# Performance work log

Hardware: AMD Instinct MI355X
Metric: run time of the kernel (lower is better)

Reference implementation:

```python
import jax, jax.numpy as jnp
import numpy as np

B, Lq, Lk, D, H = 8, 1024, 1024, 1024, 16
HD = D // H  # 64


def rotate_half(x):
    x1, x2 = jnp.split(x, 2, axis=-1)
    return jnp.concatenate([-x2, x1], axis=-1)


def setup_inputs() -> dict:
    key = jax.random.key(0)
    ks = jax.random.split(key, 16)
    inv_freq = 1.0 / (10000.0 ** (np.arange(0, HD, 2, dtype=np.float32) / HD))
    pos = np.arange(Lk, dtype=np.float32)
    ang = pos[:, None] * inv_freq[None, :]              # [Lk, HD/2]
    emb = np.concatenate([ang, ang], axis=-1)           # [Lk, HD]
    rope_cos = jnp.broadcast_to(jnp.asarray(np.cos(emb)), (B, Lk, HD))
    rope_sin = jnp.broadcast_to(jnp.asarray(np.sin(emb)), (B, Lk, HD))
    w = lambda k: jax.random.normal(k, (D, D), jnp.float32) * 0.02
    return {
        "query": jax.random.normal(ks[0], (B, Lq, D), jnp.float32),
        "key": jax.random.normal(ks[1], (B, Lk, D), jnp.float32),
        "value": jax.random.normal(ks[2], (B, Lk, D), jnp.float32),
        "Wq": w(ks[3]), "bq": jnp.zeros((D,), jnp.float32),
        "Wk": w(ks[4]), "bk": jnp.zeros((D,), jnp.float32),
        "Wv": w(ks[5]), "bv": jnp.zeros((D,), jnp.float32),
        "Wg": w(ks[6]), "bg": jnp.ones((D,), jnp.float32),
        "Wo": w(ks[7]), "bo": jnp.zeros((D,), jnp.float32),
        "rope_cos": rope_cos,
        "rope_sin": rope_sin,
        "key_padding_mask": jnp.zeros((B, Lk), bool),  # True = padded
    }


def reference(query, key, value, Wq, bq, Wk, bk, Wv, bv, Wg, bg, Wo, bo,
              rope_cos, rope_sin, key_padding_mask):
    b, lq, d = query.shape
    lk = key.shape[1]
    h, hd = H, d // H

    def heads(x, L):  # [B,L,D] -> [B,H,L,hd]
        return x.reshape(b, L, h, hd).transpose(0, 2, 1, 3)

    Q = heads(query @ Wq.T + bq, lq)
    K = heads(key @ Wk.T + bk, lk)
    V = heads(value @ Wv.T + bv, lk)

    def rope(x, cos, sin):
        L = x.shape[2]
        c = cos[:, None, :L, :]
        s = sin[:, None, :L, :]
        return x * c + rotate_half(x) * s

    K = rope(K, rope_cos, rope_sin)
    Q = rope(Q, rope_cos, rope_sin)  # rope_on_q=True, q uses same cos/sin

    scale = 1.0 / np.sqrt(hd)
    scores = jnp.einsum('bhqd,bhkd->bhqk', Q, K) * scale
    valid = ~key_padding_mask                     # [B,Lk], True = attend
    scores = jnp.where(valid[:, None, None, :], scores, jnp.float32(-1e30))
    attn = jax.nn.softmax(scores, axis=-1)
    out = jnp.einsum('bhqk,bhkd->bhqd', attn, V)  # [B,H,Lq,hd]
    out = jnp.nan_to_num(out, nan=0.0)
    out = out.transpose(0, 2, 1, 3).reshape(b, lq, d)
    gate = jax.nn.sigmoid(query @ Wg.T + bg)
    out = (out * gate) @ Wo.T + bo
    return out
```

## Files before the change

kernel.cpp:

```cpp
#include <hip/hip_runtime.h>

using ushort  = unsigned short;
using bf16x8  = __attribute__((ext_vector_type(8))) __bf16;
using bf16x4  = __attribute__((ext_vector_type(4))) __bf16;
using ushort8 = __attribute__((ext_vector_type(8))) unsigned short;
using f32x4   = __attribute__((ext_vector_type(4))) float;
using float4v = __attribute__((ext_vector_type(4))) float;

__device__ __forceinline__ float bf2f(ushort u) {
    union { unsigned int i; float f; } v; v.i = ((unsigned int)u) << 16; return v.f;
}
__device__ __forceinline__ ushort f2bf(float f) {
    union { float f; unsigned int i; } v; v.f = f;
    unsigned int r = v.i + 0x7FFFu + ((v.i >> 16) & 1u);
    return (ushort)(r >> 16);
}
__device__ __forceinline__ bf16x8 ld8(const ushort* p) {
    return __builtin_bit_cast(bf16x8, *(const ushort8*)p);
}
__device__ __forceinline__ void glds16(const void* g, void* l) {
    __builtin_amdgcn_global_load_lds(
        (const __attribute__((address_space(1))) unsigned int*)g,
        (__attribute__((address_space(3))) unsigned int*)l, 16, 0, 0);
}

__global__ void sniff_kernel(const ushort* __restrict__ q, int* __restrict__ flag) {
    const int lane = threadIdx.x;
    float mx = 0.0f;
    for (int i = lane; i < 512; i += 64) {
        float v = bf2f(q[2 * i]);
        mx = fmaxf(mx, fabsf(v));
    }
#pragma unroll
    for (int off = 32; off >= 1; off >>= 1) mx = fmaxf(mx, __shfl_xor(mx, off, 64));
    if (lane == 0) *flag = (mx > 1.0e6f) ? 1 : 0;
}

__device__ __forceinline__ void cvt8(const void* src, ushort* dst, int i, bool f32m) {
    if (f32m) {
        const float4v a = ((const float4v*)src)[2 * i];
        const float4v b = ((const float4v*)src)[2 * i + 1];
        bf16x8 o;
#pragma unroll
        for (int j = 0; j < 4; ++j) { o[j] = (__bf16)a[j]; o[j + 4] = (__bf16)b[j]; }
        ((ushort8*)dst)[i] = __builtin_bit_cast(ushort8, o);
    } else {
        ((ushort8*)dst)[i] = ((const ushort8*)src)[i];
    }
}

__global__ __launch_bounds__(256) void cvt_qkv(
    const void* __restrict__ s0, const void* __restrict__ s1, const void* __restrict__ s2,
    ushort* __restrict__ d0, ushort* __restrict__ d1, ushort* __restrict__ d2,
    const int* __restrict__ flag)
{
    const bool f32m = (*flag != 0);
    const int seg = blockIdx.x >> 11;
    const void* src = seg == 0 ? s0 : (seg == 1 ? s1 : s2);
    ushort*    dst = seg == 0 ? d0 : (seg == 1 ? d1 : d2);
    for (int i = (blockIdx.x & 2047) * 256 + threadIdx.x; i < 1048576; i += 2048 * 256)
        cvt8(src, dst, i, f32m);
}
__global__ __launch_bounds__(256) void cvt_w5(
    const void* __restrict__ s0, const void* __restrict__ s1, const void* __restrict__ s2,
    const void* __restrict__ s3, const void* __restrict__ s4,
    ushort* __restrict__ d0, ushort* __restrict__ d1, ushort* __restrict__ d2,
    ushort* __restrict__ d3, ushort* __restrict__ d4,
    const int* __restrict__ flag)
{
    const bool f32m = (*flag != 0);
    const int seg = blockIdx.x >> 9;
    const void* src = seg == 0 ? s0 : seg == 1 ? s1 : seg == 2 ? s2 : seg == 3 ? s3 : s4;
    ushort*    dst = seg == 0 ? d0 : seg == 1 ? d1 : seg == 2 ? d2 : seg == 3 ? d3 : d4;
    cvt8(src, dst, (blockIdx.x & 511) * 256 + threadIdx.x, f32m);
}

#define CHUNK_SWZ(r, s) ((s) ^ (((r) >> 1) & 3))

template<int EPI, int ABF16, int WBF16, int OUTF>
__global__ __launch_bounds__(256) void gemm_bt(
    const void* __restrict__ A, const void* __restrict__ W,
    const void* __restrict__ bias,
    const void* __restrict__ rc, const void* __restrict__ rs,
    void* __restrict__ C, const int* __restrict__ flag)
{
    constexpr int Kd = 1024, Nd = 1024;
    const bool f32m = (*flag != 0);
    const bool af32 = f32m && !ABF16;
    const bool wf32 = f32m && !WBF16;

    const int tid  = threadIdx.x;
    const int swz  = (blockIdx.x & 7) * 64 + (blockIdx.x >> 3);
    const int nb   = swz & 7;
    const int mb   = swz >> 3;
    const int wave = tid >> 6;
    const int lane = tid & 63;
    const int quad = lane >> 4;
    const int l16  = lane & 15;
    const int wr   = wave >> 1;
    const int wc   = wave & 1;

    __shared__ __align__(16) ushort As[2][128 * 32];
    __shared__ __align__(16) ushort Bs[2][128 * 32];

    const int arow0 = mb * 128;
    const int brow0 = nb * 128;

    auto ldregs = [&](float4v r[4], const float* src, int row0, int k0) {
#pragma unroll
        for (int j = 0; j < 2; ++j) {
            const int c = j * 256 + tid;
            const float* gp = src + (size_t)(row0 + (c >> 2)) * Kd + k0 + (c & 3) * 8;
            r[2 * j]     = *(const float4v*)gp;
            r[2 * j + 1] = *(const float4v*)(gp + 4);
        }
    };
    auto cvtwr = [&](ushort* lds, const float4v r[4]) {
#pragma unroll
        for (int j = 0; j < 2; ++j) {
            const int c = j * 256 + tid;
            const int row = c >> 2;
            const int sl  = CHUNK_SWZ(row, c & 3);
            bf16x8 o;
#pragma unroll
            for (int i = 0; i < 4; ++i) {
                o[i]     = (__bf16)r[2 * j][i];
                o[i + 4] = (__bf16)r[2 * j + 1][i];
            }
            *(ushort8*)&lds[row * 32 + sl * 8] = __builtin_bit_cast(ushort8, o);
        }
    };
    auto stage16 = [&](ushort* lds, const ushort* src, int row0, int k0) {
#pragma unroll
        for (int j = 0; j < 2; ++j) {
            const int t = j * 256 + tid;
            const int row = t >> 2;
            const int c   = CHUNK_SWZ(row, t & 3);
            glds16(src + (size_t)(row0 + row) * Kd + k0 + c * 8, &lds[t * 8]);
        }
    };

    {
        float4v t[4];
        if (af32) { ldregs(t, (const float*)A, arow0, 0); cvtwr(As[0], t); }
        else      stage16(As[0], (const ushort*)A, arow0, 0);
        if (wf32) { ldregs(t, (const float*)W, brow0, 0); cvtwr(Bs[0], t); }
        else      stage16(Bs[0], (const ushort*)W, brow0, 0);
    }

    f32x4 acc[4][4] = {};
    int cur = 0;
    for (int kt = 0; kt < 32; ++kt) {
        __syncthreads();
        const bool pf = (kt < 31);
        const int  kn = (kt + 1) * 32;
        float4v ra[4], rb[4];
        if (pf) {
            if (af32) ldregs(ra, (const float*)A, arow0, kn);
            else      stage16(As[cur ^ 1], (const ushort*)A, arow0, kn);
            if (wf32) ldregs(rb, (const float*)W, brow0, kn);
            else      stage16(Bs[cur ^ 1], (const ushort*)W, brow0, kn);
        }
        bf16x8 fa[4], fb[4];
#pragma unroll
        for (int mi = 0; mi < 4; ++mi) {
            const int row = wr * 64 + mi * 16 + l16;
            fa[mi] = ld8(&As[cur][row * 32 + CHUNK_SWZ(row, quad) * 8]);
        }
#pragma unroll
        for (int ni = 0; ni < 4; ++ni) {
            const int row = wc * 64 + ni * 16 + l16;
            fb[ni] = ld8(&Bs[cur][row * 32 + CHUNK_SWZ(row, quad) * 8]);
        }
#pragma unroll
        for (int mi = 0; mi < 4; ++mi)
#pragma unroll
            for (int ni = 0; ni < 4; ++ni)
                acc[mi][ni] = __builtin_amdgcn_mfma_f32_16x16x32_bf16(fa[mi], fb[ni], acc[mi][ni], 0, 0, 0);
        if (pf) {
            if (af32) cvtwr(As[cur ^ 1], ra);
            if (wf32) cvtwr(Bs[cur ^ 1], rb);
        }
        cur ^= 1;
    }

    const bool of32 = OUTF && f32m;
    const int colbase = nb * 128 + wc * 64;
    float bv[4];
#pragma unroll
    for (int ni = 0; ni < 4; ++ni) {
        const int cg = colbase + ni * 16 + l16;
        bv[ni] = f32m ? ((const float*)bias)[cg] : bf2f(((const ushort*)bias)[cg]);
    }
    const int rowb = mb * 128 + wr * 64 + quad * 4;
#pragma unroll
    for (int mi = 0; mi < 4; ++mi) {
#pragma unroll
        for (int r = 0; r < 4; ++r) {
            const int rowg = rowb + mi * 16 + r;
            float v[4];
#pragma unroll
            for (int ni = 0; ni < 4; ++ni) v[ni] = acc[mi][ni][r] + bv[ni];
            if constexpr (EPI == 1 || EPI == 3) {
#pragma unroll
                for (int t = 0; t < 2; ++t) {
                    const size_t ci = (size_t)rowg * 64 + t * 16 + l16;
                    const float c = f32m ? ((const float*)rc)[ci] : bf2f(((const ushort*)rc)[ci]);
                    const float s = f32m ? ((const float*)rs)[ci] : bf2f(((const ushort*)rs)[ci]);
                    const float x1 = v[t], x2 = v[t + 2];
                    v[t]     = x1 * c - x2 * s;
                    v[t + 2] = x2 * c + x1 * s;
                }
                if constexpr (EPI == 3) {
#pragma unroll
                    for (int t = 0; t < 4; ++t) v[t] *= 0.125f;
                }
            } else if constexpr (EPI == 2) {
#pragma unroll
                for (int t = 0; t < 4; ++t) v[t] = 1.0f / (1.0f + __expf(-v[t]));
            }
#pragma unroll
            for (int ni = 0; ni < 4; ++ni) {
                const size_t idx = (size_t)rowg * Nd + colbase + ni * 16 + l16;
                if (of32) ((float*)C)[idx] = v[ni];
                else      ((ushort*)C)[idx] = f2bf(v[ni]);
            }
        }
    }
}

__global__ __launch_bounds__(256) void gemm_qkvg(
    const ushort* __restrict__ qbf, const ushort* __restrict__ kbf,
    const ushort* __restrict__ vbf, const ushort* __restrict__ Wcat,
    const void* __restrict__ bq, const void* __restrict__ bk,
    const void* __restrict__ bv_, const void* __restrict__ bg,
    const void* __restrict__ rc, const void* __restrict__ rs,
    ushort* __restrict__ Qp, ushort* __restrict__ Kp,
    ushort* __restrict__ Vp, ushort* __restrict__ Gt,
    const int* __restrict__ flag)
{
    constexpr int Kd = 1024;
    const bool f32m = (*flag != 0);
    const int tid  = threadIdx.x;
    const int xcd  = blockIdx.x & 7;
    const int rr   = blockIdx.x >> 3;
    const int mb   = xcd * 8 + (rr & 7);
    const int nb   = rr >> 3;
    const int seg  = nb >> 3;
    const ushort* A   = seg == 0 ? qbf : seg == 1 ? kbf : seg == 2 ? vbf : qbf;
    const void* bias  = seg == 0 ? bq : seg == 1 ? bk : seg == 2 ? bv_ : bg;
    ushort* C         = seg == 0 ? Qp : seg == 1 ? Kp : seg == 2 ? Vp : Gt;

    const int wave = tid >> 6;
    const int lane = tid & 63;
    const int quad = lane >> 4;
    const int l16  = lane & 15;
    const int wr   = wave >> 1;
    const int wc   = wave & 1;

    __shared__ __align__(16) ushort As[2][128 * 32];
    __shared__ __align__(16) ushort Bs[2][128 * 32];

    const int arow0 = mb * 128;
    const int brow0 = nb * 128;

    auto stage16 = [&](ushort* lds, const ushort* src, int row0, int k0) {
#pragma unroll
        for (int j = 0; j < 2; ++j) {
            const int t = j * 256 + tid;
            const int row = t >> 2;
            const int c   = CHUNK_SWZ(row, t & 3);
            glds16(src + (size_t)(row0 + row) * Kd + k0 + c * 8, &lds[t * 8]);
        }
    };

    stage16(As[0], A, arow0, 0);
    stage16(Bs[0], Wcat, brow0, 0);

    f32x4 acc[4][4] = {};
    int cur = 0;
    for (int kt = 0; kt < 32; ++kt) {
        __syncthreads();
        if (kt < 31) {
            const int kn = (kt + 1) * 32;
            stage16(As[cur ^ 1], A, arow0, kn);
            stage16(Bs[cur ^ 1], Wcat, brow0, kn);
        }
        bf16x8 fa[4], fb[4];
#pragma unroll
        for (int mi = 0; mi < 4; ++mi) {
            const int row = wr * 64 + mi * 16 + l16;
            fa[mi] = ld8(&As[cur][row * 32 + CHUNK_SWZ(row, quad) * 8]);
        }
#pragma unroll
        for (int ni = 0; ni < 4; ++ni) {
            const int row = wc * 64 + ni * 16 + l16;
            fb[ni] = ld8(&Bs[cur][row * 32 + CHUNK_SWZ(row, quad) * 8]);
        }
#pragma unroll
        for (int mi = 0; mi < 4; ++mi)
#pragma unroll
            for (int ni = 0; ni < 4; ++ni)
                acc[mi][ni] = __builtin_amdgcn_mfma_f32_16x16x32_bf16(fa[mi], fb[ni], acc[mi][ni], 0, 0, 0);
        cur ^= 1;
    }

    const int colbase = (nb & 7) * 128 + wc * 64;
    float bv[4];
#pragma unroll
    for (int ni = 0; ni < 4; ++ni) {
        const int cg = colbase + ni * 16 + l16;
        bv[ni] = f32m ? ((const float*)bias)[cg] : bf2f(((const ushort*)bias)[cg]);
    }
    const int rowb = mb * 128 + wr * 64 + quad * 4;
#pragma unroll
    for (int mi = 0; mi < 4; ++mi) {
#pragma unroll
        for (int r = 0; r < 4; ++r) {
            const int rowg = rowb + mi * 16 + r;
            float v[4];
#pragma unroll
            for (int ni = 0; ni < 4; ++ni) v[ni] = acc[mi][ni][r] + bv[ni];
            if (seg <= 1) {
#pragma unroll
                for (int t = 0; t < 2; ++t) {
                    const size_t ci = (size_t)rowg * 64 + t * 16 + l16;
                    const float c = f32m ? ((const float*)rc)[ci] : bf2f(((const ushort*)rc)[ci]);
                    const float s = f32m ? ((const float*)rs)[ci] : bf2f(((const ushort*)rs)[ci]);
                    const float x1 = v[t], x2 = v[t + 2];
                    v[t]     = x1 * c - x2 * s;
                    v[t + 2] = x2 * c + x1 * s;
                }
                if (seg == 0) {
#pragma unroll
                    for (int t = 0; t < 4; ++t) v[t] *= 0.125f;
                }
            } else if (seg == 3) {
#pragma unroll
                for (int t = 0; t < 4; ++t) v[t] = 1.0f / (1.0f + __expf(-v[t]));
            }
#pragma unroll
            for (int ni = 0; ni < 4; ++ni) {
                const size_t idx = (size_t)rowg * 1024 + colbase + ni * 16 + l16;
                C[idx] = f2bf(v[ni]);
            }
        }
    }
}

__global__ __launch_bounds__(256) void transpose_vh(
    const ushort* __restrict__ Vp, ushort* __restrict__ Vt)
{
    const int bb = blockIdx.x >> 8;
    const int pr = (blockIdx.x >> 4) & 15;
    const int cr = blockIdx.x & 15;
    __shared__ ushort t[64 * 65];
    const int tid = threadIdx.x;
    {
        const int r = tid >> 3, c8 = (tid & 7) * 8;
#pragma unroll
        for (int hh = 0; hh < 2; ++hh) {
            const int rr = r + hh * 32;
            const ushort8 v = *(const ushort8*)(Vp + ((size_t)(bb * 1024 + pr * 64 + rr)) * 1024 + cr * 64 + c8);
#pragma unroll
            for (int i = 0; i < 8; ++i) t[rr * 65 + c8 + i] = v[i];
        }
    }
    __syncthreads();
    {
        const int c = tid >> 2, p0 = (tid & 3) * 16;
        ushort8 o0, o1;
#pragma unroll
        for (int i = 0; i < 8; ++i) {
            o0[i] = t[(p0 + i) * 65 + c];
            o1[i] = t[(p0 + 8 + i) * 65 + c];
        }
        ushort* dst = Vt + ((size_t)(bb * 1024 + cr * 64 + c)) * 1024 + pr * 64 + p0;
        *(ushort8*)dst       = o0;
        *(ushort8*)(dst + 8) = o1;
    }
}

__global__ __launch_bounds__(512) void attn_kernel(
    const ushort* __restrict__ Qp, const ushort* __restrict__ Kp,
    const ushort* __restrict__ Vt, const ushort* __restrict__ G,
    const unsigned char* __restrict__ mask, ushort* __restrict__ O)
{
    const int swz = (blockIdx.x & 7) * 64 + (blockIdx.x >> 3);
    const int qb = swz & 3;
    const int h  = (swz >> 2) & 15;
    const int b  = swz >> 6;
    const int tid  = threadIdx.x;
    const int wave = tid >> 6;
    const int lane = tid & 63;
    const int quad = lane >> 4;
    const int l16  = lane & 15;
    const size_t Dm = 1024;

    __shared__ __align__(16) ushort Ks[2][64 * 64];
    __shared__ __align__(16) ushort Vs[2][64 * 64];
    __shared__ __align__(16) ushort Ps[8][2][16 * 72];
    __shared__ __align__(16) unsigned char Ms[1024];

    const int q0 = qb * 256 + wave * 32;
    bf16x8 qa[2][2];
#pragma unroll
    for (int u = 0; u < 2; ++u) {
        const ushort* Qb = Qp + ((size_t)b * 1024 + q0 + u * 16 + l16) * Dm + h * 64 + quad * 8;
        qa[u][0] = ld8(Qb);
        qa[u][1] = ld8(Qb + 32);
    }
    const ushort* Kbase = Kp + ((size_t)b * 1024) * Dm + h * 64;
    const ushort* Vbase = Vt + ((size_t)b * 1024 + h * 64) * 1024;

    auto stageK = [&](ushort* lds, int k0) {
        const int row = tid >> 3;
        const int col8 = (tid & 7) ^ (row & 7);
        glds16(Kbase + (size_t)(k0 + row) * Dm + col8 * 8, &lds[tid * 8]);
    };
    auto stageV = [&](ushort* lds, int k0) {
        const int row = tid >> 3;
        const int col8 = (tid & 7) ^ (row & 7);
        glds16(Vbase + (size_t)row * 1024 + k0 + col8 * 8, &lds[tid * 8]);
    };

    stageK(Ks[0], 0);
    stageV(Vs[0], 0);
    if (tid < 256)
        ((unsigned int*)Ms)[tid] = ((const unsigned int*)(mask + (size_t)b * 1024))[tid];
    __syncthreads();
    bool anym;
    {
        const unsigned long long* M8 = (const unsigned long long*)Ms;
        anym = __any((M8[lane] | M8[lane + 64]) != 0ULL);
    }

    float m_r[2] = { -3.0e38f, -3.0e38f };
    float l_r[2] = { 0.0f, 0.0f };
    f32x4 o[2][4] = {};

    int cur = 0;
    for (int kt = 0; kt < 16; ++kt) {
        __syncthreads();
        if (kt < 15) {
            stageK(Ks[cur ^ 1], (kt + 1) * 64);
            stageV(Vs[cur ^ 1], (kt + 1) * 64);
        }
        const int k0 = kt * 64;
        bf16x8 kf0[4], kf1[4];
#pragma unroll
        for (int ct = 0; ct < 4; ++ct) {
            const int row = ct * 16 + l16;
            kf0[ct] = ld8(&Ks[cur][row * 64 + ((quad)     ^ (row & 7)) * 8]);
            kf1[ct] = ld8(&Ks[cur][row * 64 + ((4 + quad) ^ (row & 7)) * 8]);
        }
        f32x4 s[2][4] = {};
        __builtin_amdgcn_s_setprio(1);
#pragma unroll
        for (int u = 0; u < 2; ++u)
#pragma unroll
            for (int ct = 0; ct < 4; ++ct) {
                s[u][ct] = __builtin_amdgcn_mfma_f32_16x16x32_bf16(kf0[ct], qa[u][0], s[u][ct], 0, 0, 0);
                s[u][ct] = __builtin_amdgcn_mfma_f32_16x16x32_bf16(kf1[ct], qa[u][1], s[u][ct], 0, 0, 0);
            }
        __builtin_amdgcn_s_setprio(0);
        bf16x8 vf[4][2];
#pragma unroll
        for (int t = 0; t < 4; ++t) {
            const int row = t * 16 + l16;
#pragma unroll
            for (int kk = 0; kk < 2; ++kk)
                vf[t][kk] = ld8(&Vs[cur][row * 64 + (((kk * 4 + quad) ^ (row & 7))) * 8]);
        }
#pragma unroll
        for (int u = 0; u < 2; ++u) {
            float sv[4][4];
#pragma unroll
            for (int ct = 0; ct < 4; ++ct)
#pragma unroll
                for (int r = 0; r < 4; ++r) sv[ct][r] = s[u][ct][r];
            if (anym) {
#pragma unroll
                for (int ct = 0; ct < 4; ++ct) {
                    const unsigned int mb4 = *(const unsigned int*)&Ms[k0 + ct * 16 + quad * 4];
#pragma unroll
                    for (int r = 0; r < 4; ++r)
                        if ((mb4 >> (8 * r)) & 0xffu) sv[ct][r] = -1e30f;
                }
            }
            float mxv = sv[0][0];
#pragma unroll
            for (int ct = 0; ct < 4; ++ct)
#pragma unroll
                for (int r = 0; r < 4; ++r) mxv = fmaxf(mxv, sv[ct][r]);
            mxv = fmaxf(mxv, __shfl_xor(mxv, 16, 64));
            mxv = fmaxf(mxv, __shfl_xor(mxv, 32, 64));
            if (__any(mxv > m_r[u] + 8.0f)) {
                const float mnew  = fmaxf(m_r[u], mxv);
                const float alpha = __expf(m_r[u] - mnew);
                l_r[u] *= alpha;
                m_r[u]  = mnew;
#pragma unroll
                for (int r = 0; r < 4; ++r) {
                    const float ar = __shfl(alpha, quad * 4 + r, 64);
#pragma unroll
                    for (int t = 0; t < 4; ++t) o[u][t][r] *= ar;
                }
            }
            float ls = 0.0f;
            bf16x4 w[4];
#pragma unroll
            for (int ct = 0; ct < 4; ++ct)
#pragma unroll
                for (int r = 0; r < 4; ++r) {
                    const float pv = __expf(sv[ct][r] - m_r[u]);
                    ls += pv;
                    w[ct][r] = (__bf16)pv;
                }
            l_r[u] += ls;
#pragma unroll
            for (int ct = 0; ct < 4; ++ct)
                *(bf16x4*)&Ps[wave][u][l16 * 72 + ct * 16 + quad * 4] = w[ct];
        }
        asm volatile("s_waitcnt lgkmcnt(0)" ::: "memory");
        __builtin_amdgcn_sched_barrier(0);
        bf16x8 pa[2][2];
#pragma unroll
        for (int u = 0; u < 2; ++u) {
            pa[u][0] = ld8(&Ps[wave][u][l16 * 72 + quad * 8]);
            pa[u][1] = ld8(&Ps[wave][u][l16 * 72 + 32 + quad * 8]);
        }
        __builtin_amdgcn_s_setprio(1);
#pragma unroll
        for (int u = 0; u < 2; ++u)
#pragma unroll
            for (int t = 0; t < 4; ++t) {
                o[u][t] = __builtin_amdgcn_mfma_f32_16x16x32_bf16(pa[u][0], vf[t][0], o[u][t], 0, 0, 0);
                o[u][t] = __builtin_amdgcn_mfma_f32_16x16x32_bf16(pa[u][1], vf[t][1], o[u][t], 0, 0, 0);
            }
        __builtin_amdgcn_s_setprio(0);
        cur ^= 1;
    }
#pragma unroll
    for (int u = 0; u < 2; ++u) {
        float lt = l_r[u];
        lt += __shfl_xor(lt, 16, 64);
        lt += __shfl_xor(lt, 32, 64);
        const int rowg0 = b * 1024 + q0 + u * 16 + quad * 4;
#pragma unroll
        for (int r = 0; r < 4; ++r) {
            const float inv = 1.0f / __shfl(lt, quad * 4 + r, 64);
#pragma unroll
            for (int t = 0; t < 4; ++t) {
                const size_t idx = (size_t)(rowg0 + r) * Dm + h * 64 + t * 16 + l16;
                O[idx] = f2bf(o[u][t][r] * inv * bf2f(G[idx]));
            }
        }
    }
}

extern "C" void kernel_launch(void* const* d_in, const int* in_sizes, int n_in,
                              void* d_out, int out_size, void* d_ws, size_t ws_size,
                              hipStream_t stream)
{
    const void* query = d_in[0];
    const void* key   = d_in[1];
    const void* value = d_in[2];
    const void* Wq    = d_in[3];
    const void* bq    = d_in[4];
    const void* Wk    = d_in[5];
    const void* bk    = d_in[6];
    const void* Wv    = d_in[7];
    const void* bv    = d_in[8];
    const void* Wg    = d_in[9];
    const void* bg    = d_in[10];
    const void* Wo    = d_in[11];
    const void* bo    = d_in[12];
    const void* rc    = d_in[13];
    const void* rs    = d_in[14];
    const unsigned char* mask = (const unsigned char*)d_in[15];

    char* ws = (char*)d_ws;
    const size_t MB = (size_t)1 << 20;
    const size_t MB16 = 16 * MB;
    const bool big = ws_size >= 139 * MB;

    ushort* Qp = (ushort*)(ws);
    ushort* Kp = (ushort*)(ws + 1 * MB16);
    ushort* Vp = (ushort*)(ws + 2 * MB16);
    ushort* Gt = (ushort*)(ws + 3 * MB16);
    ushort* Vt = (ushort*)(ws + 4 * MB16);
    ushort* Ag = (ushort*)(ws + 2 * MB16);
    int*  flag = (int*)(ws + (big ? 138 * MB : 5 * MB16));

    const dim3 gb(512), gt(256);
    hipLaunchKernelGGL(sniff_kernel, dim3(1), dim3(64), 0, stream, (const ushort*)query, flag);

    if (big) {
        ushort* qbf = (ushort*)(ws + 80 * MB);
        ushort* kbf = (ushort*)(ws + 96 * MB);
        ushort* vbf = (ushort*)(ws + 112 * MB);
        ushort* wcat = (ushort*)(ws + 128 * MB);
        ushort* wb[5];
        for (int i = 0; i < 5; ++i) wb[i] = wcat + (size_t)i * 1024 * 1024;

        hipLaunchKernelGGL(cvt_qkv, dim3(3 * 2048), dim3(256), 0, stream,
                           query, key, value, qbf, kbf, vbf, flag);
        hipLaunchKernelGGL(cvt_w5, dim3(5 * 512), dim3(256), 0, stream,
                           Wq, Wk, Wv, Wg, Wo, wb[0], wb[1], wb[2], wb[3], wb[4], flag);

        hipLaunchKernelGGL(gemm_qkvg, dim3(2048), dim3(256), 0, stream,
                           qbf, kbf, vbf, wcat, bq, bk, bv, bg, rc, rs,
                           Qp, Kp, Vp, Gt, flag);

        hipLaunchKernelGGL(transpose_vh, dim3(2048), dim3(256), 0, stream, Vp, Vt);
        hipLaunchKernelGGL(attn_kernel,  dim3(512), dim3(512), 0, stream, Qp, Kp, Vt, Gt, mask, Ag);

        hipLaunchKernelGGL((gemm_bt<0,1,1,1>), gb, gt, 0, stream, Ag, wb[4], bo, rc, rs, d_out, flag);
    } else {
        hipLaunchKernelGGL((gemm_bt<3,0,0,0>), gb, gt, 0, stream, query, Wq, bq, rc, rs, Qp, flag);
        hipLaunchKernelGGL((gemm_bt<1,0,0,0>), gb, gt, 0, stream, key,   Wk, bk, rc, rs, Kp, flag);
        hipLaunchKernelGGL((gemm_bt<0,0,0,0>), gb, gt, 0, stream, value, Wv, bv, rc, rs, Vp, flag);
        hipLaunchKernelGGL((gemm_bt<2,0,0,0>), gb, gt, 0, stream, query, Wg, bg, rc, rs, Gt, flag);

        hipLaunchKernelGGL(transpose_vh, dim3(2048), dim3(256), 0, stream, Vp, Vt);
        hipLaunchKernelGGL(attn_kernel,  dim3(512), dim3(512), 0, stream, Qp, Kp, Vt, Gt, mask, Ag);

        hipLaunchKernelGGL((gemm_bt<0,1,0,1>), gb, gt, 0, stream, Ag, Wo, bo, rc, rs, d_out, flag);
    }
}
```

Before: 387.9 us.

## Fuse V transpose into QKVG GEMM epilogue and shrink attention blocks

The V-projection tiles of the fused QKVG GEMM now transpose through shared memory in the epilogue and write straight into the head-transposed Vt layout. This removes the separate transpose_vh launch and its extra global round trip. Separately, the attention kernel moves from 512-thread blocks over 256 queries to 256-thread blocks over 128 queries, doubling the grid to 1024 blocks. That raises block count and occupancy flexibility, but each block now restages K/V tiles for fewer queries.

```diff
diff --git a/kernel.cpp b/kernel.cpp
--- a/kernel.cpp
+++ b/kernel.cpp
@@ -236,7 +236,7 @@
     const void* __restrict__ bv_, const void* __restrict__ bg,
     const void* __restrict__ rc, const void* __restrict__ rs,
     ushort* __restrict__ Qp, ushort* __restrict__ Kp,
-    ushort* __restrict__ Vp, ushort* __restrict__ Gt,
+    ushort* __restrict__ Vt, ushort* __restrict__ Gt,
     const int* __restrict__ flag)
 {
     constexpr int Kd = 1024;
@@ -247,9 +247,9 @@
     const int mb   = xcd * 8 + (rr & 7);
     const int nb   = rr >> 3;
     const int seg  = nb >> 3;
-    const ushort* A   = seg == 0 ? qbf : seg == 1 ? kbf : seg == 2 ? vbf : qbf;
-    const void* bias  = seg == 0 ? bq : seg == 1 ? bk : seg == 2 ? bv_ : bg;
-    ushort* C         = seg == 0 ? Qp : seg == 1 ? Kp : seg == 2 ? Vp : Gt;
+    const ushort* A = seg == 0 ? qbf : seg == 1 ? kbf : seg == 2 ? vbf : qbf;
+    const void* bias = seg == 0 ? bq : seg == 1 ? bk : seg == 2 ? bv_ : bg;
+    ushort* C        = seg == 0 ? Qp : seg == 1 ? Kp : seg == 2 ? Vt : Gt;
 
     const int wave = tid >> 6;
     const int lane = tid & 63;
@@ -258,8 +258,7 @@
     const int wr   = wave >> 1;
     const int wc   = wave & 1;
 
-    __shared__ __align__(16) ushort As[2][128 * 32];
-    __shared__ __align__(16) ushort Bs[2][128 * 32];
+    __shared__ __align__(16) ushort SM[4][128 * 32];
 
     const int arow0 = mb * 128;
     const int brow0 = nb * 128;
@@ -274,8 +273,8 @@
         }
     };
 
-    stage16(As[0], A, arow0, 0);
-    stage16(Bs[0], Wcat, brow0, 0);
+    stage16(SM[0], A, arow0, 0);
+    stage16(SM[2], Wcat, brow0, 0);
 
     f32x4 acc[4][4] = {};
     int cur = 0;
@@ -283,19 +282,19 @@
         __syncthreads();
         if (kt < 31) {
             const int kn = (kt + 1) * 32;
-            stage16(As[cur ^ 1], A, arow0, kn);
-            stage16(Bs[cur ^ 1], Wcat, brow0, kn);
+            stage16(SM[cur ^ 1], A, arow0, kn);
+            stage16(SM[2 + (cur ^ 1)], Wcat, brow0, kn);
         }
         bf16x8 fa[4], fb[4];
 #pragma unroll
         for (int mi = 0; mi < 4; ++mi) {
             const int row = wr * 64 + mi * 16 + l16;
-            fa[mi] = ld8(&As[cur][row * 32 + CHUNK_SWZ(row, quad) * 8]);
+            fa[mi] = ld8(&SM[cur][row * 32 + CHUNK_SWZ(row, quad) * 8]);
         }
 #pragma unroll
         for (int ni = 0; ni < 4; ++ni) {
             const int row = wc * 64 + ni * 16 + l16;
-            fb[ni] = ld8(&Bs[cur][row * 32 + CHUNK_SWZ(row, quad) * 8]);
+            fb[ni] = ld8(&SM[2 + cur][row * 32 + CHUNK_SWZ(row, quad) * 8]);
         }
 #pragma unroll
         for (int mi = 0; mi < 4; ++mi)
@@ -312,6 +311,42 @@
         const int cg = colbase + ni * 16 + l16;
         bv[ni] = f32m ? ((const float*)bias)[cg] : bf2f(((const ushort*)bias)[cg]);
     }
+
+    if (seg == 2) {
+        ushort* TB = &SM[0][0];
+        const int bb    = mb >> 3;
+        const int pbase = (mb & 7) * 128;
+        const int cbase = (nb & 7) * 128;
+#pragma unroll
+        for (int p = 0; p < 2; ++p) {
+            __syncthreads();
+            if (wr == p) {
+#pragma unroll
+                for (int mi = 0; mi < 4; ++mi)
+#pragma unroll
+                    for (int r = 0; r < 4; ++r) {
+                        const int lr = mi * 16 + quad * 4 + r;
+#pragma unroll
+                        for (int ni = 0; ni < 4; ++ni)
+                            TB[lr * 132 + wc * 64 + ni * 16 + l16] =
+                                f2bf(acc[mi][ni][r] + bv[ni]);
+                    }
+            }
+            __syncthreads();
+            const int c = tid >> 1;
+            ushort* dst = Vt + ((size_t)(bb * 1024 + cbase + c)) * 1024 + pbase + p * 64;
+#pragma unroll
+            for (int j = 0; j < 4; ++j) {
+                const int p0 = (tid & 1) * 32 + j * 8;
+                ushort8 o8;
+#pragma unroll
+                for (int i = 0; i < 8; ++i) o8[i] = TB[(p0 + i) * 132 + c];
+                *(ushort8*)(dst + p0) = o8;
+            }
+        }
+        return;
+    }
+
     const int rowb = mb * 128 + wr * 64 + quad * 4;
 #pragma unroll
     for (int mi = 0; mi < 4; ++mi) {
@@ -335,7 +370,7 @@
 #pragma unroll
                     for (int t = 0; t < 4; ++t) v[t] *= 0.125f;
                 }
-            } else if (seg == 3) {
+            } else {
 #pragma unroll
                 for (int t = 0; t < 4; ++t) v[t] = 1.0f / (1.0f + __expf(-v[t]));
             }
@@ -381,15 +416,15 @@
     }
 }
 
-__global__ __launch_bounds__(512) void attn_kernel(
+__global__ __launch_bounds__(256) void attn_kernel(
     const ushort* __restrict__ Qp, const ushort* __restrict__ Kp,
     const ushort* __restrict__ Vt, const ushort* __restrict__ G,
     const unsigned char* __restrict__ mask, ushort* __restrict__ O)
 {
-    const int swz = (blockIdx.x & 7) * 64 + (blockIdx.x >> 3);
-    const int qb = swz & 3;
-    const int h  = (swz >> 2) & 15;
-    const int b  = swz >> 6;
+    const int swz = (blockIdx.x & 7) * 128 + (blockIdx.x >> 3);
+    const int qb = swz & 7;
+    const int h  = (swz >> 3) & 15;
+    const int b  = swz >> 7;
     const int tid  = threadIdx.x;
     const int wave = tid >> 6;
     const int lane = tid & 63;
@@ -399,10 +434,10 @@
 
     __shared__ __align__(16) ushort Ks[2][64 * 64];
     __shared__ __align__(16) ushort Vs[2][64 * 64];
-    __shared__ __align__(16) ushort Ps[8][2][16 * 72];
+    __shared__ __align__(16) ushort Ps[4][2][16 * 72];
     __shared__ __align__(16) unsigned char Ms[1024];
 
-    const int q0 = qb * 256 + wave * 32;
+    const int q0 = qb * 128 + wave * 32;
     bf16x8 qa[2][2];
 #pragma unroll
     for (int u = 0; u < 2; ++u) {
@@ -414,20 +449,27 @@
     const ushort* Vbase = Vt + ((size_t)b * 1024 + h * 64) * 1024;
 
     auto stageK = [&](ushort* lds, int k0) {
-        const int row = tid >> 3;
-        const int col8 = (tid & 7) ^ (row & 7);
-        glds16(Kbase + (size_t)(k0 + row) * Dm + col8 * 8, &lds[tid * 8]);
+#pragma unroll
+        for (int j = 0; j < 2; ++j) {
+            const int t = j * 256 + tid;
+            const int row = t >> 3;
+            const int col8 = (t & 7) ^ (row & 7);
+            glds16(Kbase + (size_t)(k0 + row) * Dm + col8 * 8, &lds[t * 8]);
+        }
     };
     auto stageV = [&](ushort* lds, int k0) {
-        const int row = tid >> 3;
-        const int col8 = (tid & 7) ^ (row & 7);
-        glds16(Vbase + (size_t)row * 1024 + k0 + col8 * 8, &lds[tid * 8]);
+#pragma unroll
+        for (int j = 0; j < 2; ++j) {
+            const int t = j * 256 + tid;
+            const int row = t >> 3;
+            const int col8 = (t & 7) ^ (row & 7);
+            glds16(Vbase + (size_t)row * 1024 + k0 + col8 * 8, &lds[t * 8]);
+        }
     };
 
     stageK(Ks[0], 0);
     stageV(Vs[0], 0);
-    if (tid < 256)
-        ((unsigned int*)Ms)[tid] = ((const unsigned int*)(mask + (size_t)b * 1024))[tid];
+    ((unsigned int*)Ms)[tid] = ((const unsigned int*)(mask + (size_t)b * 1024))[tid];
     __syncthreads();
     bool anym;
     {
@@ -611,10 +653,9 @@
 
         hipLaunchKernelGGL(gemm_qkvg, dim3(2048), dim3(256), 0, stream,
                            qbf, kbf, vbf, wcat, bq, bk, bv, bg, rc, rs,
-                           Qp, Kp, Vp, Gt, flag);
-
-        hipLaunchKernelGGL(transpose_vh, dim3(2048), dim3(256), 0, stream, Vp, Vt);
-        hipLaunchKernelGGL(attn_kernel,  dim3(512), dim3(512), 0, stream, Qp, Kp, Vt, Gt, mask, Ag);
+                           Qp, Kp, Vt, Gt, flag);
+
+        hipLaunchKernelGGL(attn_kernel, dim3(1024), dim3(256), 0, stream, Qp, Kp, Vt, Gt, mask, Ag);
 
         hipLaunchKernelGGL((gemm_bt<0,1,1,1>), gb, gt, 0, stream, Ag, wb[4], bo, rc, rs, d_out, flag);
     } else {
@@ -624,7 +665,7 @@
         hipLaunchKernelGGL((gemm_bt<2,0,0,0>), gb, gt, 0, stream, query, Wg, bg, rc, rs, Gt, flag);
 
         hipLaunchKernelGGL(transpose_vh, dim3(2048), dim3(256), 0, stream, Vp, Vt);
-        hipLaunchKernelGGL(attn_kernel,  dim3(512), dim3(512), 0, stream, Qp, Kp, Vt, Gt, mask, Ag);
+        hipLaunchKernelGGL(attn_kernel,  dim3(1024), dim3(256), 0, stream, Qp, Kp, Vt, Gt, mask, Ag);
 
         hipLaunchKernelGGL((gemm_bt<0,1,0,1>), gb, gt, 0, stream, Ag, Wo, bo, rc, rs, d_out, flag);
     }
```

Result: no change. 388.3 us (+0.1%).
